# Kernel optimization log

Measured on AMD Instinct MI355X. Metric: run time of the kernel, lower is better.

Reference implementation:

```python
import jax, jax.numpy as jnp
import numpy as np

EPS_NORM = 1e-8
EPS_SIGN = 1e-6


def _renorm(s):
    n = jnp.maximum(jnp.linalg.norm(s, axis=-1, keepdims=True), EPS_NORM)
    return s / n


def setup_inputs() -> dict:
    key = jax.random.key(0)
    k1, k2, k3 = jax.random.split(key, 3)
    B, T, D = 8, 4096, 1024
    x = jax.random.normal(k1, (B, T, D), dtype=jnp.float32)
    tape_init = jax.random.normal(k2, (D,), dtype=jnp.float32) / np.sqrt(D)
    eta = jnp.float32(0.1)
    torque_bias = jax.random.normal(k3, (D,), dtype=jnp.float32) * 0.01
    return {"x": x, "tape_init": tape_init, "eta": eta, "torque_bias": torque_bias}


def reference(x, tape_init, eta, torque_bias):
    B, T, D = x.shape
    s0 = _renorm(jnp.broadcast_to(tape_init[None, :], (B, D)))  # (B, D)
    eta_abs = jnp.abs(eta)

    def step(s, h):
        c = h * s
        res = (c > EPS_SIGN).astype(x.dtype)
        tor = (c < -EPS_SIGN).astype(x.dtype)
        orth = 1.0 - res - tor
        update = eta_abs * (c * (1.0 - orth) + tor * torque_bias)
        s_new = _renorm(s + update)
        return s_new, s_new

    # scan over time: xs shaped (T, B, D)
    _, outs = jax.lax.scan(step, s0, jnp.swapaxes(x, 0, 1))
    return jnp.swapaxes(outs, 0, 1)  # (B, T, D)
```

## Files before the change

kernel.cpp:

```cpp
#include <hip/hip_runtime.h>
#include <math.h>

#define EPS_NORM_F 1e-8f
#define EPS_SIGN_F 1e-6f

struct alignas(16) F4v { float a0, a1, a2, a3; };

template <int CTRL>
__device__ __forceinline__ float dpp_add(float v) {
  int p = __builtin_amdgcn_update_dpp(0, __float_as_int(v), CTRL, 0xF, 0xF, true);
  return v + __int_as_float(p);
}

__device__ __forceinline__ float wave_sum(float ps) {
  ps = dpp_add<0xB1>(ps);
  ps = dpp_add<0x4E>(ps);
  ps = dpp_add<0x141>(ps);
  ps = dpp_add<0x140>(ps);
  ps = dpp_add<0x142>(ps);
  ps = dpp_add<0x143>(ps);
  return ps;
}

__device__ __forceinline__ void sync_lds() {
  asm volatile("s_waitcnt lgkmcnt(0)" ::: "memory");
  __builtin_amdgcn_s_barrier();
  asm volatile("" ::: "memory");
}

__global__ __launch_bounds__(256) void me_scan(
    const float* __restrict__ x,
    const float* __restrict__ tape_init,
    const float* __restrict__ eta_p,
    const float* __restrict__ tb_p,
    float* __restrict__ out,
    int T, int D) {
  const int tid  = threadIdx.x;
  const int lane = tid & 63;
  const int wid  = tid >> 6;
  const int d0   = tid << 2;
  const int b    = blockIdx.x;

  __shared__ __align__(16) float red[2][4];

  const float eta_abs = fabsf(eta_p[0]);
  const F4v tb = *(const F4v*)(tb_p + d0);

  const float* xb = x   + (size_t)b * (size_t)T * (size_t)D;
  float*       ob = out + (size_t)b * (size_t)T * (size_t)D;

  float s0, s1, s2, s3;

  {
    F4v ti = *(const F4v*)(tape_init + d0);
    s0 = ti.a0; s1 = ti.a1; s2 = ti.a2; s3 = ti.a3;
    float ps = wave_sum((s0 * s0 + s1 * s1) + (s2 * s2 + s3 * s3));
    if (lane == 63) red[0][wid] = ps;
    sync_lds();
    F4v r = *(const F4v*)(&red[0][0]);
    float S = (r.a0 + r.a1) + (r.a2 + r.a3);
    float n = fmaxf(sqrtf(S), EPS_NORM_F);
    float inv = 1.0f / n;
    s0 *= inv; s1 *= inv; s2 *= inv; s3 *= inv;
  }

  F4v ha = *(const F4v*)(xb + d0);
  F4v hb = *(const F4v*)(xb + (size_t)D + d0);

  #pragma unroll 2
  for (int t = 0; t < T; ++t) {
    const int tn = (t + 2 < T) ? (t + 2) : (T - 1);
    F4v hc = *(const F4v*)(xb + (size_t)tn * (size_t)D + d0);

    float u0, u1, u2, u3;
    {
      float c;
      c = ha.a0 * s0;
      u0 = s0 + eta_abs * (((fabsf(c) > EPS_SIGN_F) ? c : 0.0f) + ((c < -EPS_SIGN_F) ? tb.a0 : 0.0f));
      c = ha.a1 * s1;
      u1 = s1 + eta_abs * (((fabsf(c) > EPS_SIGN_F) ? c : 0.0f) + ((c < -EPS_SIGN_F) ? tb.a1 : 0.0f));
      c = ha.a2 * s2;
      u2 = s2 + eta_abs * (((fabsf(c) > EPS_SIGN_F) ? c : 0.0f) + ((c < -EPS_SIGN_F) ? tb.a2 : 0.0f));
      c = ha.a3 * s3;
      u3 = s3 + eta_abs * (((fabsf(c) > EPS_SIGN_F) ? c : 0.0f) + ((c < -EPS_SIGN_F) ? tb.a3 : 0.0f));
    }

    float ps = wave_sum((u0 * u0 + u1 * u1) + (u2 * u2 + u3 * u3));
    const int slot = (t + 1) & 1;
    if (lane == 63) red[slot][wid] = ps;
    sync_lds();
    F4v r = *(const F4v*)(&red[slot][0]);
    float S = (r.a0 + r.a1) + (r.a2 + r.a3);

    float n = fmaxf(sqrtf(S), EPS_NORM_F);
    float inv = 1.0f / n;

    s0 = u0 * inv; s1 = u1 * inv; s2 = u2 * inv; s3 = u3 * inv;

    F4v sv; sv.a0 = s0; sv.a1 = s1; sv.a2 = s2; sv.a3 = s3;
    *(F4v*)(ob + (size_t)t * (size_t)D + d0) = sv;

    ha = hb; hb = hc;
  }
}

extern "C" void kernel_launch(void* const* d_in, const int* in_sizes, int n_in,
                              void* d_out, int out_size, void* d_ws, size_t ws_size,
                              hipStream_t stream) {
  const float* x         = (const float*)d_in[0];
  const float* tape_init = (const float*)d_in[1];
  const float* eta       = (const float*)d_in[2];
  const float* tbias     = (const float*)d_in[3];
  float* out = (float*)d_out;

  const int D = in_sizes[1];
  const int B = 8;
  const int T = in_sizes[0] / (B * D);

  dim3 grid(B), block(D / 4);
  hipLaunchKernelGGL(me_scan, grid, block, 0, stream,
                     x, tape_init, eta, tbias, out, T, D);
}
```

Before: 2.243 ms.

## Use single wavefront per batch row to drop LDS barrier reduction

New measurement: 1.799 ms. -19.8%, faster.

```diff
diff --git a/kernel.cpp b/kernel.cpp
--- a/kernel.cpp
+++ b/kernel.cpp
@@ -4,7 +4,7 @@
 #define EPS_NORM_F 1e-8f
 #define EPS_SIGN_F 1e-6f
 
-struct alignas(16) F4v { float a0, a1, a2, a3; };
+struct alignas(16) F4 { float v0, v1, v2, v3; };
 
 template <int CTRL>
 __device__ __forceinline__ float dpp_add(float v) {
@@ -12,95 +12,125 @@
   return v + __int_as_float(p);
 }
 
-__device__ __forceinline__ float wave_sum(float ps) {
+__device__ __forceinline__ float wave_sum_bcast(float ps) {
   ps = dpp_add<0xB1>(ps);
   ps = dpp_add<0x4E>(ps);
   ps = dpp_add<0x141>(ps);
   ps = dpp_add<0x140>(ps);
   ps = dpp_add<0x142>(ps);
   ps = dpp_add<0x143>(ps);
-  return ps;
+  return __int_as_float(__builtin_amdgcn_readlane(__float_as_int(ps), 63));
 }
 
-__device__ __forceinline__ void sync_lds() {
-  asm volatile("s_waitcnt lgkmcnt(0)" ::: "memory");
-  __builtin_amdgcn_s_barrier();
-  asm volatile("" ::: "memory");
-}
-
-__global__ __launch_bounds__(256) void me_scan(
+__global__ __launch_bounds__(64) void me_scan(
     const float* __restrict__ x,
     const float* __restrict__ tape_init,
     const float* __restrict__ eta_p,
     const float* __restrict__ tb_p,
     float* __restrict__ out,
-    int T, int D) {
-  const int tid  = threadIdx.x;
-  const int lane = tid & 63;
-  const int wid  = tid >> 6;
-  const int d0   = tid << 2;
+    int T) {
+  const int lane = threadIdx.x;
   const int b    = blockIdx.x;
-
-  __shared__ __align__(16) float red[2][4];
+  const int D    = 1024;
 
   const float eta_abs = fabsf(eta_p[0]);
-  const F4v tb = *(const F4v*)(tb_p + d0);
 
-  const float* xb = x   + (size_t)b * (size_t)T * (size_t)D;
-  float*       ob = out + (size_t)b * (size_t)T * (size_t)D;
+  float etb[4][4];
+  {
+    const F4* tbp = (const F4*)tb_p;
+#pragma unroll
+    for (int k = 0; k < 4; ++k) {
+      F4 t4 = tbp[k * 64 + lane];
+      etb[k][0] = eta_abs * t4.v0; etb[k][1] = eta_abs * t4.v1;
+      etb[k][2] = eta_abs * t4.v2; etb[k][3] = eta_abs * t4.v3;
+    }
+  }
 
-  float s0, s1, s2, s3;
+  const float* xb = x   + (size_t)b * (size_t)T * D;
+  float*       ob = out + (size_t)b * (size_t)T * D;
+
+  float v[4][4];
+  float thr, inv;
 
   {
-    F4v ti = *(const F4v*)(tape_init + d0);
-    s0 = ti.a0; s1 = ti.a1; s2 = ti.a2; s3 = ti.a3;
-    float ps = wave_sum((s0 * s0 + s1 * s1) + (s2 * s2 + s3 * s3));
-    if (lane == 63) red[0][wid] = ps;
-    sync_lds();
-    F4v r = *(const F4v*)(&red[0][0]);
-    float S = (r.a0 + r.a1) + (r.a2 + r.a3);
+    const F4* tip = (const F4*)tape_init;
+    float acc[4];
+#pragma unroll
+    for (int k = 0; k < 4; ++k) {
+      F4 t4 = tip[k * 64 + lane];
+      v[k][0] = t4.v0; v[k][1] = t4.v1; v[k][2] = t4.v2; v[k][3] = t4.v3;
+      acc[k] = (t4.v0 * t4.v0 + t4.v1 * t4.v1) + (t4.v2 * t4.v2 + t4.v3 * t4.v3);
+    }
+    float S = wave_sum_bcast((acc[0] + acc[1]) + (acc[2] + acc[3]));
     float n = fmaxf(sqrtf(S), EPS_NORM_F);
-    float inv = 1.0f / n;
-    s0 *= inv; s1 *= inv; s2 *= inv; s3 *= inv;
+    float r = 1.0f / n;
+#pragma unroll
+    for (int k = 0; k < 4; ++k)
+#pragma unroll
+      for (int j = 0; j < 4; ++j) v[k][j] *= r;
+    inv = 1.0f;
+    thr = EPS_SIGN_F;
   }
 
-  F4v ha = *(const F4v*)(xb + d0);
-  F4v hb = *(const F4v*)(xb + (size_t)D + d0);
+  F4 h[4][4];
+#pragma unroll
+  for (int i = 0; i < 4; ++i) {
+    const F4* xr = (const F4*)(xb + (size_t)((i < T) ? i : (T - 1)) * D);
+#pragma unroll
+    for (int k = 0; k < 4; ++k) h[i][k] = xr[k * 64 + lane];
+  }
 
-  #pragma unroll 2
-  for (int t = 0; t < T; ++t) {
-    const int tn = (t + 2 < T) ? (t + 2) : (T - 1);
-    F4v hc = *(const F4v*)(xb + (size_t)tn * (size_t)D + d0);
+  for (int tt = 0; tt < T; tt += 4) {
+#pragma unroll
+    for (int i = 0; i < 4; ++i) {
+      const int t = tt + i;
 
-    float u0, u1, u2, u3;
-    {
-      float c;
-      c = ha.a0 * s0;
-      u0 = s0 + eta_abs * (((fabsf(c) > EPS_SIGN_F) ? c : 0.0f) + ((c < -EPS_SIGN_F) ? tb.a0 : 0.0f));
-      c = ha.a1 * s1;
-      u1 = s1 + eta_abs * (((fabsf(c) > EPS_SIGN_F) ? c : 0.0f) + ((c < -EPS_SIGN_F) ? tb.a1 : 0.0f));
-      c = ha.a2 * s2;
-      u2 = s2 + eta_abs * (((fabsf(c) > EPS_SIGN_F) ? c : 0.0f) + ((c < -EPS_SIGN_F) ? tb.a2 : 0.0f));
-      c = ha.a3 * s3;
-      u3 = s3 + eta_abs * (((fabsf(c) > EPS_SIGN_F) ? c : 0.0f) + ((c < -EPS_SIGN_F) ? tb.a3 : 0.0f));
+      float cc[4][4];
+#pragma unroll
+      for (int k = 0; k < 4; ++k) {
+        cc[k][0] = h[i][k].v0 * v[k][0];
+        cc[k][1] = h[i][k].v1 * v[k][1];
+        cc[k][2] = h[i][k].v2 * v[k][2];
+        cc[k][3] = h[i][k].v3 * v[k][3];
+      }
+      {
+        const int tn = (t + 4 < T) ? (t + 4) : (T - 1);
+        const F4* xr = (const F4*)(xb + (size_t)tn * D);
+#pragma unroll
+        for (int k = 0; k < 4; ++k) h[i][k] = xr[k * 64 + lane];
+      }
+      float acc[4];
+#pragma unroll
+      for (int k = 0; k < 4; ++k) {
+        float a = 0.0f;
+#pragma unroll
+        for (int j = 0; j < 4; ++j) {
+          float c  = cc[k][j];
+          float cm = (fabsf(c) > thr) ? c : 0.0f;
+          float bb = (c < -thr) ? etb[k][j] : 0.0f;
+          float w  = fmaf(eta_abs, cm, v[k][j]);
+          float xn = fmaf(inv, w, bb);
+          v[k][j]  = xn;
+          a = fmaf(xn, xn, a);
+        }
+        acc[k] = a;
+      }
+      float S = wave_sum_bcast((acc[0] + acc[1]) + (acc[2] + acc[3]));
+      float n = fmaxf(sqrtf(S), EPS_NORM_F);
+      float r = 1.0f / n;
+      thr = EPS_SIGN_F * n;
+      {
+        F4* orow = (F4*)(ob + (size_t)t * D);
+#pragma unroll
+        for (int k = 0; k < 4; ++k) {
+          F4 o;
+          o.v0 = v[k][0] * r; o.v1 = v[k][1] * r;
+          o.v2 = v[k][2] * r; o.v3 = v[k][3] * r;
+          orow[k * 64 + lane] = o;
+        }
+      }
+      inv = r;
     }
-
-    float ps = wave_sum((u0 * u0 + u1 * u1) + (u2 * u2 + u3 * u3));
-    const int slot = (t + 1) & 1;
-    if (lane == 63) red[slot][wid] = ps;
-    sync_lds();
-    F4v r = *(const F4v*)(&red[slot][0]);
-    float S = (r.a0 + r.a1) + (r.a2 + r.a3);
-
-    float n = fmaxf(sqrtf(S), EPS_NORM_F);
-    float inv = 1.0f / n;
-
-    s0 = u0 * inv; s1 = u1 * inv; s2 = u2 * inv; s3 = u3 * inv;
-
-    F4v sv; sv.a0 = s0; sv.a1 = s1; sv.a2 = s2; sv.a3 = s3;
-    *(F4v*)(ob + (size_t)t * (size_t)D + d0) = sv;
-
-    ha = hb; hb = hc;
   }
 }
 
@@ -113,11 +143,11 @@
   const float* tbias     = (const float*)d_in[3];
   float* out = (float*)d_out;
 
-  const int D = in_sizes[1];
+  const int D = 1024;
   const int B = 8;
   const int T = in_sizes[0] / (B * D);
 
-  dim3 grid(B), block(D / 4);
+  dim3 grid(B), block(64);
   hipLaunchKernelGGL(me_scan, grid, block, 0, stream,
-                     x, tape_init, eta, tbias, out, T, D);
+                     x, tape_init, eta, tbias, out, T);
 }
```
